# Performance work log

Hardware: AMD Instinct MI355X
Metric: run time of the kernel (lower is better)

## Reference

```python
import jax, jax.numpy as jnp
import numpy as np

N = 10000        # nodes
E = 160000       # edges (avg degree 16)
C = 64           # hidden channels
L = 2            # interaction/product/readout blocks
NTYPES = 5       # len(atomic_numbers)
NB = 8           # Bessel radial basis size
G = 100          # graphs in batch
R_MAX = 5.0
AVG_NEI = 16.0   # avg_num_neighbors normalization
LM = 9           # (l_max+1)^2, l_max=2


def _spherical_harmonics(u):
    # real spherical harmonics up to l=2 of unit vectors u [E,3] -> [E,9]
    x, y, z = u[:, 0], u[:, 1], u[:, 2]
    s3 = 1.7320508
    one = jnp.ones_like(x)
    return jnp.stack([
        one,                       # l=0
        x, y, z,                   # l=1
        s3 * x * y,                # l=2
        s3 * y * z,
        0.5 * (3.0 * z * z - 1.0),
        s3 * x * z,
        0.5 * s3 * (x * x - y * y),
    ], axis=-1)


def _radial_embedding(r):
    # Bessel basis * polynomial cutoff (p=6); r [E] -> [E,NB]
    r_safe = jnp.maximum(r, 1e-9)
    n = jnp.arange(1, NB + 1, dtype=r.dtype)
    pref = jnp.sqrt(jnp.asarray(2.0 / R_MAX, r.dtype))
    bessel = pref * jnp.sin(n[None, :] * jnp.pi * r[:, None] / R_MAX) / r_safe[:, None]
    xx = r / R_MAX
    env = 1.0 - 28.0 * xx**6 + 48.0 * xx**7 - 21.0 * xx**8
    env = jnp.where(xx < 1.0, env, 0.0)
    return bessel * env[:, None]


def setup_inputs() -> dict:
    key = jax.random.key(0)
    ks = jax.random.split(key, 14)
    sc = 0.1
    return {
        'pos': jax.random.normal(ks[0], (N, 3), jnp.float32),
        'W_embed': jax.random.normal(ks[1], (NTYPES, C), jnp.float32) * sc,
        'W_r1': jax.random.normal(ks[2], (NB, 64), jnp.float32) * sc,
        'b_r1': jnp.zeros((64,), jnp.float32),
        'W_r2': jax.random.normal(ks[3], (64, C), jnp.float32) * sc,
        'W_up': jax.random.normal(ks[4], (L, C, C), jnp.float32) * sc,
        'W_sc': jax.random.normal(ks[5], (L, C, C), jnp.float32) * sc,
        'W_prod': jax.random.normal(ks[6], (L, C, C), jnp.float32) * sc,
        'w_ro': jax.random.normal(ks[7], (L, C, 1), jnp.float32) * sc,
        'atom_types': jax.random.randint(ks[8], (N,), 0, NTYPES),
        'edge_index': jax.random.randint(ks[9], (2, E), 0, N),
        'batch': jnp.sort(jax.random.randint(ks[10], (N,), 0, G)),
        'num_graphs': G,
    }


def reference(pos, W_embed, W_r1, b_r1, W_r2, W_up, W_sc, W_prod, w_ro,
              atom_types, edge_index, batch, num_graphs):
    node_attrs = jax.nn.one_hot(atom_types, NTYPES, dtype=pos.dtype)   # [N,5]
    h = node_attrs @ W_embed                                           # [N,C]

    sender, receiver = edge_index[0], edge_index[1]
    vec = pos[receiver] - pos[sender]                                  # edge gather
    r = jnp.linalg.norm(vec, axis=-1)                                  # [E]
    u = vec / jnp.maximum(r, 1e-9)[:, None]
    sh = _spherical_harmonics(u)                                       # [E,LM]
    ef = _radial_embedding(r)                                          # [E,NB]
    R = jax.nn.silu(ef @ W_r1 + b_r1) @ W_r2                            # [E,C] radial MLP

    pair_energy = jnp.zeros((num_graphs,), pos.dtype)                  # no pair_repulsion_fn
    energies = [pair_energy]
    for l in range(L):
        h1 = h @ W_up[l]                                               # [N,C]
        # tensor-product message: outer(sh_e, R_e * h_sender)  [E,LM,C]
        m = sh[:, :, None] * (R * h1[sender])[:, None, :]
        A = jax.ops.segment_sum(m, receiver, num_segments=N) / AVG_NEI  # [N,LM,C]
        sc = h @ W_sc[l]                                               # skip connection
        # product basis: l=0 channel + quadratic invariant contraction
        q = A[:, 0, :] + jnp.sum(A * A, axis=1)                         # [N,C]
        h = q @ W_prod[l] + sc
        node_e = (h @ w_ro[l])[:, 0]                                    # [N]
        energies.append(jax.ops.segment_sum(node_e, batch, num_segments=num_graphs))

    contributions = jnp.stack(energies, axis=-1)                        # [G, L+1]
    total_energy = jnp.sum(contributions, axis=-1)                      # [G]
    return total_energy
```

## Files before the change

### kernel.cpp

```cpp
#include <hip/hip_runtime.h>
#include <hip/hip_fp16.h>
#include <math.h>

#define Nn 10000
#define Ee 160000
#define NBb 8
#define Gg 100
#define NT 5
#define CSRMAX 230400
#define EDGEBLK (CSRMAX / 256)

__device__ __align__(16) float g_shc[(size_t)CSRMAX * 12];
__device__ __align__(16) __half2 g_R2[(size_t)(CSRMAX / 2) * 64];
__device__ float g_h1a[Nn * 64];
__device__ float g_h1b[Nn * 64];
__device__ float g_hscb[Nn * 64];
__device__ float g_nodeE[2][Nn];
__device__ int   g_deg[Nn];
__device__ int   g_offs[Nn + 1];
__device__ int   g_cursor[Nn];
__device__ int2  g_er[CSRMAX];
__device__ float g_W1T[64 * NBb];
__device__ float g_E1[NT * 64];
__device__ float g_Esc[NT * 64];
__device__ float g_T1[NT * 64];
__device__ float g_T2[NT * 64];
__device__ float g_M12[64 * 128];
__device__ float g_wp0ro[64];
__device__ float g_wpro[64];
__device__ float g_t0[NT];

__global__ __launch_bounds__(256) void k_init(const float* __restrict__ Wr1,
                                              const float* __restrict__ Wembed,
                                              const float* __restrict__ Wup,
                                              const float* __restrict__ Wsc,
                                              const float* __restrict__ Wprod,
                                              const float* __restrict__ wro,
                                              float* __restrict__ out, int out_size) {
    int t = threadIdx.x;
    int b = blockIdx.x;
    if (b >= 17) {
        int i = (b - 17) * 256 + t;
        if (i < CSRMAX) g_er[i].x = -1;
        if (i < out_size) out[i] = 0.0f;
        if (i < Nn) { g_deg[i] = 0; g_cursor[i] = 0; }
        return;
    }
    if (b == 0) {
        for (int i = t; i < 64 * NBb; i += 256) {
            int k = i >> 6, j = i & 63;
            g_W1T[j * NBb + k] = Wr1[i];
        }
        for (int i = t; i < NT * 64; i += 256) {
            int g = i >> 6, c = i & 63;
            float s1 = 0.f, s2 = 0.f;
            for (int j = 0; j < 64; j++) {
                float w = Wembed[g * 64 + j];
                s1 += w * Wup[j * 64 + c];
                s2 += w * Wsc[j * 64 + c];
            }
            g_E1[i] = s1; g_Esc[i] = s2;
        }
        if (t < 64) {
            float s1 = 0.f, s2 = 0.f;
            for (int c = 0; c < 64; c++) {
                s1 += Wprod[t * 64 + c] * wro[c];
                s2 += Wprod[4096 + t * 64 + c] * wro[64 + c];
            }
            g_wp0ro[t] = s1; g_wpro[t] = s2;
        }
        __syncthreads();
        for (int i = t; i < NT * 64; i += 256) {
            int g = i >> 6, c = i & 63;
            float s1 = 0.f, s2 = 0.f;
            for (int j = 0; j < 64; j++) {
                float w = g_Esc[g * 64 + j];
                s1 += w * Wup[4096 + j * 64 + c];
                s2 += w * Wsc[4096 + j * 64 + c];
            }
            g_T1[i] = s1; g_T2[i] = s2;
        }
        if (t < NT) {
            float s = 0.f;
            for (int j = 0; j < 64; j++) s += g_Esc[t * 64 + j] * wro[j];
            g_t0[t] = s;
        }
    } else {
        int idx = (b - 1) * 256 + t;
        int k = idx >> 6, c = idx & 63;
        float s1 = 0.f, s2 = 0.f;
        for (int j = 0; j < 64; j++) {
            float w = Wprod[k * 64 + j];
            s1 += w * Wup[4096 + j * 64 + c];
            s2 += w * Wsc[4096 + j * 64 + c];
        }
        g_M12[k * 128 + c] = s1;
        g_M12[k * 128 + 64 + c] = s2;
    }
}

__global__ __launch_bounds__(256) void k_deg(const int* __restrict__ eidx) {
    int e = blockIdx.x * 256 + threadIdx.x;
    if (e < Ee) atomicAdd(&g_deg[eidx[Ee + e]], 1);
}

__global__ __launch_bounds__(1024) void k_scan() {
    __shared__ int part[1024];
    int t = threadIdx.x;
    const int CH = (Nn + 1023) / 1024;
    int st = t * CH;
    int en = st + CH; if (en > Nn) en = Nn;
    int s = 0;
    for (int i = st; i < en; i++) s += (g_deg[i] + 7) & ~7;
    part[t] = s;
    __syncthreads();
    for (int d = 1; d < 1024; d <<= 1) {
        int v = (t >= d) ? part[t - d] : 0;
        __syncthreads();
        part[t] += v;
        __syncthreads();
    }
    int base = (t == 0) ? 0 : part[t - 1];
    for (int i = st; i < en; i++) { g_offs[i] = base; base += (g_deg[i] + 7) & ~7; }
    if (t == 1023) g_offs[Nn] = part[1023];
}

__global__ __launch_bounds__(256) void k_fill(const int* __restrict__ eidx) {
    int e = blockIdx.x * 256 + threadIdx.x;
    if (e >= Ee) return;
    int snd = eidx[e];
    int r = eidx[Ee + e];
    int p = g_offs[r] + atomicAdd(&g_cursor[r], 1);
    g_er[p] = make_int2(snd, r);
}

__global__ __launch_bounds__(512) void k_edge(const float* __restrict__ pos,
                                              const float* __restrict__ br1,
                                              const float* __restrict__ Wr2,
                                              const int* __restrict__ atom_types) {
    int t = threadIdx.x;
    if (blockIdx.x >= EDGEBLK) {
        int i = (blockIdx.x - EDGEBLK) * 512 + t;
        if (i < Nn * 64) {
            int n = i >> 6, c = i & 63;
            g_h1a[i] = g_E1[atom_types[n] * 64 + c];
        }
        return;
    }
    __shared__ float sT[32][257];
    int total = g_offs[Nn];
    if (blockIdx.x * 256 >= total) return;
    int slot = t & 255;
    int chalf = __builtin_amdgcn_readfirstlane(t >> 8);
    int s = blockIdx.x * 256 + slot;
    int2 er = g_er[s];
    bool real = (er.x >= 0);
    int snd = real ? er.x : 0;
    int rcv = real ? er.y : 0;

    float vx = pos[3 * rcv + 0] - pos[3 * snd + 0];
    float vy = pos[3 * rcv + 1] - pos[3 * snd + 1];
    float vz = pos[3 * rcv + 2] - pos[3 * snd + 2];
    float r = sqrtf(vx * vx + vy * vy + vz * vz);
    float inv = __builtin_amdgcn_rcpf(fmaxf(r, 1e-9f));
    float x = vx * inv, y = vy * inv, z = vz * inv;
    const float s3 = 1.7320508f;
    if (chalf == 0) {
        float4* shp = (float4*)(g_shc + (size_t)s * 12);
        if (real) {
            shp[0] = make_float4(1.0f, x, y, z);
            shp[1] = make_float4(s3 * x * y, s3 * y * z, 0.5f * (3.0f * z * z - 1.0f), s3 * x * z);
            shp[2] = make_float4(0.5f * s3 * (x * x - y * y), __int_as_float(snd), 0.f, 0.f);
        } else {
            shp[0] = make_float4(0.f, 0.f, 0.f, 0.f);
            shp[1] = make_float4(0.f, 0.f, 0.f, 0.f);
            shp[2] = make_float4(0.f, 0.f, 0.f, 0.f);
        }
    }

    float xx = r * 0.2f;
    float env = 0.0f;
    if (xx < 1.0f) {
        float x2 = xx * xx;
        float x6 = x2 * x2 * x2;
        float x7 = x6 * xx;
        float x8 = x7 * xx;
        env = 1.0f - 28.0f * x6 + 48.0f * x7 - 21.0f * x8;
    }
    const float pref = 0.63245553f;
    const float PI_F = 3.14159265358979f;
    float fac = pref * inv * env;
    float ef[NBb];
#pragma unroll
    for (int k = 0; k < NBb; k++)
        ef[k] = fac * __sinf((float)(k + 1) * PI_F * r * 0.2f);

    float acc[32];
#pragma unroll
    for (int c = 0; c < 32; c++) acc[c] = 0.0f;
    const float* __restrict__ w2base = Wr2 + chalf * 32;
    for (int j = 0; j < 64; j++) {
        float a = br1[j];
#pragma unroll
        for (int k = 0; k < NBb; k++) a += ef[k] * g_W1T[j * NBb + k];
        a = a * __builtin_amdgcn_rcpf(1.0f + __expf(-a));
        const float* __restrict__ w2 = w2base + j * 64;
#pragma unroll
        for (int c = 0; c < 32; c++) acc[c] += a * w2[c];
    }

    size_t baseP = (size_t)blockIdx.x * 128;
#pragma unroll
    for (int chunk = 0; chunk < 2; chunk++) {
        if (chalf == chunk) {
#pragma unroll
            for (int c = 0; c < 32; c++) sT[c][slot] = real ? acc[c] : 0.0f;
        }
        __syncthreads();
        {
            int p = t >> 2;
            int cg = t & 3;
            __half2 out8[8];
#pragma unroll
            for (int j = 0; j < 8; j++) {
                int c = cg * 8 + j;
                out8[j] = __floats2half2_rn(sT[c][2 * p], sT[c][2 * p + 1]);
            }
            __half2* dst = g_R2 + (baseP + p) * 64 + chunk * 32 + cg * 8;
            *(uint4*)dst = *(uint4*)out8;
        }
        __syncthreads();
    }
}

#define PROCESS_BATCH(rec, j0)                                                   \
    {                                                                            \
        __half2 r2[4];                                                           \
        _Pragma("unroll")                                                        \
        for (int kk = 0; kk < 4; kk++)                                           \
            r2[kk] = g_R2[((j0) / 2 + kk) * 64 + lane];                          \
        _Pragma("unroll")                                                        \
        for (int k = 0; k < 8; k++) {                                            \
            float s0 = __shfl(rec.x, 3 * k, 64), s1 = __shfl(rec.y, 3 * k, 64);  \
            float s2 = __shfl(rec.z, 3 * k, 64), s3 = __shfl(rec.w, 3 * k, 64);  \
            float s4 = __shfl(rec.x, 3 * k + 1, 64), s5 = __shfl(rec.y, 3 * k + 1, 64); \
            float s6 = __shfl(rec.z, 3 * k + 1, 64), s7 = __shfl(rec.w, 3 * k + 1, 64); \
            float s8 = __shfl(rec.x, 3 * k + 2, 64);                             \
            int src = __float_as_int(__shfl(rec.y, 3 * k + 2, 64));              \
            float rv = (k & 1) ? __high2float(r2[k >> 1]) : __low2float(r2[k >> 1]); \
            float tv = rv * hsrc[(size_t)src * 64 + lane];                       \
            A[0] += s0 * tv; A[1] += s1 * tv; A[2] += s2 * tv;                   \
            A[3] += s3 * tv; A[4] += s4 * tv; A[5] += s5 * tv;                   \
            A[6] += s6 * tv; A[7] += s7 * tv; A[8] += s8 * tv;                   \
        }                                                                        \
    }

__global__ __launch_bounds__(256) void k_node0(const int* __restrict__ atom_types) {
    int t = threadIdx.x;
    int node = blockIdx.x * 4 + (t >> 6);
    int lane = t & 63;
    int boff = __builtin_amdgcn_readfirstlane(g_offs[node]);
    int nb = (__builtin_amdgcn_readfirstlane(g_deg[node]) + 7) >> 3;
    const float* __restrict__ hsrc = g_h1a;
    float A[9];
#pragma unroll
    for (int m = 0; m < 9; m++) A[m] = 0.0f;
    float4 rec[4];
#pragma unroll
    for (int b = 0; b < 4; b++) {
        rec[b] = make_float4(0.f, 0.f, 0.f, 0.f);
        if (b < nb && lane < 24)
            rec[b] = *(const float4*)(g_shc + ((size_t)boff + (size_t)b * 8) * 12 + (size_t)lane * 4);
    }
#pragma unroll
    for (int b = 0; b < 4; b++)
        if (b < nb) PROCESS_BATCH(rec[b], ((size_t)boff + (size_t)b * 8));
    for (int b = 4; b < nb; b++) {
        size_t j0 = (size_t)boff + (size_t)b * 8;
        float4 rc = make_float4(0.f, 0.f, 0.f, 0.f);
        if (lane < 24) rc = *(const float4*)(g_shc + j0 * 12 + (size_t)lane * 4);
        PROCESS_BATCH(rc, j0);
    }
    const float invn = 1.0f / 16.0f;
    float q = A[0] * invn;
#pragma unroll
    for (int m = 0; m < 9; m++) {
        float a = A[m] * invn;
        q += a * a;
    }
    int type = __builtin_amdgcn_readfirstlane(atom_types[node]);
    float h1n = g_T1[type * 64 + lane];
    float hscn = g_T2[type * 64 + lane];
#pragma unroll
    for (int k = 0; k < 64; k++) {
        float qk = __shfl(q, k, 64);
        h1n += qk * g_M12[k * 128 + lane];
        hscn += qk * g_M12[k * 128 + 64 + lane];
    }
    g_h1b[node * 64 + lane] = h1n;
    g_hscb[node * 64 + lane] = hscn;
    float v = q * g_wp0ro[lane];
#pragma unroll
    for (int off = 32; off > 0; off >>= 1) v += __shfl_down(v, off, 64);
    if (lane == 0) g_nodeE[0][node] = v + g_t0[type];
}

__global__ __launch_bounds__(256) void k_node1(const float* __restrict__ wro) {
    int t = threadIdx.x;
    int node = blockIdx.x * 4 + (t >> 6);
    int lane = t & 63;
    int boff = __builtin_amdgcn_readfirstlane(g_offs[node]);
    int nb = (__builtin_amdgcn_readfirstlane(g_deg[node]) + 7) >> 3;
    const float* __restrict__ hsrc = g_h1b;
    float A[9];
#pragma unroll
    for (int m = 0; m < 9; m++) A[m] = 0.0f;
    float4 rec[4];
#pragma unroll
    for (int b = 0; b < 4; b++) {
        rec[b] = make_float4(0.f, 0.f, 0.f, 0.f);
        if (b < nb && lane < 24)
            rec[b] = *(const float4*)(g_shc + ((size_t)boff + (size_t)b * 8) * 12 + (size_t)lane * 4);
    }
#pragma unroll
    for (int b = 0; b < 4; b++)
        if (b < nb) PROCESS_BATCH(rec[b], ((size_t)boff + (size_t)b * 8));
    for (int b = 4; b < nb; b++) {
        size_t j0 = (size_t)boff + (size_t)b * 8;
        float4 rc = make_float4(0.f, 0.f, 0.f, 0.f);
        if (lane < 24) rc = *(const float4*)(g_shc + j0 * 12 + (size_t)lane * 4);
        PROCESS_BATCH(rc, j0);
    }
    const float invn = 1.0f / 16.0f;
    float q = A[0] * invn;
#pragma unroll
    for (int m = 0; m < 9; m++) {
        float a = A[m] * invn;
        q += a * a;
    }
    float v = q * g_wpro[lane] + g_hscb[node * 64 + lane] * wro[lane];
#pragma unroll
    for (int off = 32; off > 0; off >>= 1) v += __shfl_down(v, off, 64);
    if (lane == 0) g_nodeE[1][node] = v;
}

__global__ __launch_bounds__(64) void k_energy(const int* __restrict__ batch,
                                               float* __restrict__ out) {
    int g = blockIdx.x;
    int lane = threadIdx.x;
    int a = 0, b = Nn;
    while (a < b) { int m = (a + b) >> 1; if (batch[m] < g) a = m + 1; else b = m; }
    int st = a;
    b = Nn;
    while (a < b) { int m = (a + b) >> 1; if (batch[m] < g + 1) a = m + 1; else b = m; }
    int en = a;
    float s = 0.0f;
    for (int i = st + lane; i < en; i += 64) s += g_nodeE[0][i] + g_nodeE[1][i];
#pragma unroll
    for (int off = 32; off > 0; off >>= 1) s += __shfl_down(s, off, 64);
    if (lane == 0) out[g] = s;
}

extern "C" void kernel_launch(void* const* d_in, const int* in_sizes, int n_in,
                              void* d_out, int out_size, void* d_ws, size_t ws_size,
                              hipStream_t stream) {
    const float* pos     = (const float*)d_in[0];
    const float* W_embed = (const float*)d_in[1];
    const float* W_r1    = (const float*)d_in[2];
    const float* b_r1    = (const float*)d_in[3];
    const float* W_r2    = (const float*)d_in[4];
    const float* W_up    = (const float*)d_in[5];
    const float* W_sc    = (const float*)d_in[6];
    const float* W_prod  = (const float*)d_in[7];
    const float* w_ro    = (const float*)d_in[8];
    const int* atom_types = (const int*)d_in[9];
    const int* eidx       = (const int*)d_in[10];
    const int* batch      = (const int*)d_in[11];
    float* out = (float*)d_out;

    k_init<<<17 + EDGEBLK, 256, 0, stream>>>(W_r1, W_embed, W_up, W_sc, W_prod, w_ro, out, out_size);
    k_deg<<<Ee / 256, 256, 0, stream>>>(eidx);
    k_scan<<<1, 1024, 0, stream>>>();
    k_fill<<<Ee / 256, 256, 0, stream>>>(eidx);
    k_edge<<<EDGEBLK + (Nn * 64 + 511) / 512, 512, 0, stream>>>(pos, b_r1, W_r2, atom_types);
    k_node0<<<Nn / 4, 256, 0, stream>>>(atom_types);
    k_node1<<<Nn / 4, 256, 0, stream>>>(w_ro + 64);
    k_energy<<<Gg, 64, 0, stream>>>(batch, out);
}
```

Before: 223.9 us.

## Compute radial MLP second layer with MFMA f16 matrix instructions in k_edge

The second radial-MLP matmul (64x64 per edge), previously done with scalar FMAs split across two thread halves per edge, now runs on MFMA 16x16x32 f16 instructions. Hidden activations are staged in swizzled LDS as fp16 and W_r2 is transposed into LDS, and each block now uses 256 threads with one edge per thread. This cuts FP32 ALU work and drops the old transpose staging, at the cost of fp16 rounding of the hidden activations and weights plus a per-block W_r2 load into LDS.

Result: faster. 211.2 us (-5.6%).

```diff
diff --git a/kernel.cpp b/kernel.cpp
--- a/kernel.cpp
+++ b/kernel.cpp
@@ -9,6 +9,9 @@
 #define NT 5
 #define CSRMAX 230400
 #define EDGEBLK (CSRMAX / 256)
+
+typedef _Float16 half8v __attribute__((ext_vector_type(8)));
+typedef float f32x4v __attribute__((ext_vector_type(4)));
 
 __device__ __align__(16) float g_shc[(size_t)CSRMAX * 12];
 __device__ __align__(16) __half2 g_R2[(size_t)(CSRMAX / 2) * 64];
@@ -134,25 +137,28 @@
     g_er[p] = make_int2(snd, r);
 }
 
-__global__ __launch_bounds__(512) void k_edge(const float* __restrict__ pos,
+__global__ __launch_bounds__(256) void k_edge(const float* __restrict__ pos,
                                               const float* __restrict__ br1,
                                               const float* __restrict__ Wr2,
                                               const int* __restrict__ atom_types) {
     int t = threadIdx.x;
     if (blockIdx.x >= EDGEBLK) {
-        int i = (blockIdx.x - EDGEBLK) * 512 + t;
+        int i = (blockIdx.x - EDGEBLK) * 256 + t;
         if (i < Nn * 64) {
             int n = i >> 6, c = i & 63;
             g_h1a[i] = g_E1[atom_types[n] * 64 + c];
         }
         return;
     }
-    __shared__ float sT[32][257];
+    __shared__ _Float16 sA[256 * 64];
+    __shared__ _Float16 sB[64 * 64];
     int total = g_offs[Nn];
     if (blockIdx.x * 256 >= total) return;
-    int slot = t & 255;
-    int chalf = __builtin_amdgcn_readfirstlane(t >> 8);
-    int s = blockIdx.x * 256 + slot;
+
+    for (int i = t; i < 64 * 64; i += 256)
+        sB[(i & 63) * 64 + (i >> 6)] = (_Float16)Wr2[i];
+
+    int s = blockIdx.x * 256 + t;
     int2 er = g_er[s];
     bool real = (er.x >= 0);
     int snd = real ? er.x : 0;
@@ -165,7 +171,7 @@
     float inv = __builtin_amdgcn_rcpf(fmaxf(r, 1e-9f));
     float x = vx * inv, y = vy * inv, z = vz * inv;
     const float s3 = 1.7320508f;
-    if (chalf == 0) {
+    {
         float4* shp = (float4*)(g_shc + (size_t)s * 12);
         if (real) {
             shp[0] = make_float4(1.0f, x, y, z);
@@ -195,41 +201,53 @@
     for (int k = 0; k < NBb; k++)
         ef[k] = fac * __sinf((float)(k + 1) * PI_F * r * 0.2f);
 
-    float acc[32];
-#pragma unroll
-    for (int c = 0; c < 32; c++) acc[c] = 0.0f;
-    const float* __restrict__ w2base = Wr2 + chalf * 32;
-    for (int j = 0; j < 64; j++) {
-        float a = br1[j];
-#pragma unroll
-        for (int k = 0; k < NBb; k++) a += ef[k] * g_W1T[j * NBb + k];
-        a = a * __builtin_amdgcn_rcpf(1.0f + __expf(-a));
-        const float* __restrict__ w2 = w2base + j * 64;
-#pragma unroll
-        for (int c = 0; c < 32; c++) acc[c] += a * w2[c];
-    }
-
-    size_t baseP = (size_t)blockIdx.x * 128;
-#pragma unroll
-    for (int chunk = 0; chunk < 2; chunk++) {
-        if (chalf == chunk) {
-#pragma unroll
-            for (int c = 0; c < 32; c++) sT[c][slot] = real ? acc[c] : 0.0f;
-        }
-        __syncthreads();
-        {
-            int p = t >> 2;
-            int cg = t & 3;
-            __half2 out8[8];
-#pragma unroll
-            for (int j = 0; j < 8; j++) {
-                int c = cg * 8 + j;
-                out8[j] = __floats2half2_rn(sT[c][2 * p], sT[c][2 * p + 1]);
-            }
-            __half2* dst = g_R2 + (baseP + p) * 64 + chunk * 32 + cg * 8;
-            *(uint4*)dst = *(uint4*)out8;
-        }
-        __syncthreads();
+#pragma unroll
+    for (int gnl = 0; gnl < 8; gnl++) {
+        half8v h8;
+#pragma unroll
+        for (int i2 = 0; i2 < 8; i2++) {
+            int j = gnl * 8 + i2;
+            float a = br1[j];
+#pragma unroll
+            for (int k = 0; k < NBb; k++) a += ef[k] * g_W1T[j * NBb + k];
+            a = a * __builtin_amdgcn_rcpf(1.0f + __expf(-a));
+            h8[i2] = (_Float16)(real ? a : 0.0f);
+        }
+        int pg = gnl ^ (t & 7);
+        *(half8v*)&sA[t * 64 + pg * 8] = h8;
+    }
+    __syncthreads();
+
+    int lane = t & 63;
+    int w = t >> 6;
+    half8v Bf[4][2];
+#pragma unroll
+    for (int n = 0; n < 4; n++) {
+#pragma unroll
+        for (int kk = 0; kk < 2; kk++) {
+            int c = n * 16 + (lane & 15);
+            int j0 = kk * 32 + (lane >> 4) * 8;
+            Bf[n][kk] = *(const half8v*)&sB[c * 64 + j0];
+        }
+    }
+#pragma unroll
+    for (int m = 0; m < 4; m++) {
+        int row = w * 64 + m * 16 + (lane & 15);
+        int q0 = (lane >> 4) ^ (lane & 7);
+        int q1 = (4 + (lane >> 4)) ^ (lane & 7);
+        half8v A0 = *(const half8v*)&sA[row * 64 + q0 * 8];
+        half8v A1 = *(const half8v*)&sA[row * 64 + q1 * 8];
+        size_t pairbase = (size_t)blockIdx.x * 128 + (size_t)w * 32 + m * 8 + (lane >> 4) * 2;
+        int cbase = lane & 15;
+#pragma unroll
+        for (int n = 0; n < 4; n++) {
+            f32x4v d = {0.f, 0.f, 0.f, 0.f};
+            d = __builtin_amdgcn_mfma_f32_16x16x32_f16(A0, Bf[n][0], d, 0, 0, 0);
+            d = __builtin_amdgcn_mfma_f32_16x16x32_f16(A1, Bf[n][1], d, 0, 0, 0);
+            int c = n * 16 + cbase;
+            g_R2[pairbase * 64 + c]       = __floats2half2_rn(d[0], d[1]);
+            g_R2[(pairbase + 1) * 64 + c] = __floats2half2_rn(d[2], d[3]);
+        }
     }
 }
 
@@ -382,7 +400,7 @@
     k_deg<<<Ee / 256, 256, 0, stream>>>(eidx);
     k_scan<<<1, 1024, 0, stream>>>();
     k_fill<<<Ee / 256, 256, 0, stream>>>(eidx);
-    k_edge<<<EDGEBLK + (Nn * 64 + 511) / 512, 512, 0, stream>>>(pos, b_r1, W_r2, atom_types);
+    k_edge<<<EDGEBLK + (Nn * 64 + 255) / 256, 256, 0, stream>>>(pos, b_r1, W_r2, atom_types);
     k_node0<<<Nn / 4, 256, 0, stream>>>(atom_types);
     k_node1<<<Nn / 4, 256, 0, stream>>>(w_ro + 64);
     k_energy<<<Gg, 64, 0, stream>>>(batch, out);
```
